# Performance work log

Measured on AMD Instinct MI355X. Metric: run time of the kernel, lower is better.

The kernel has to match this reference:

```python
import jax, jax.numpy as jnp
import numpy as np


def _maxpool2(t):
    # 2x2 max pool, stride 2. t: [B, C, H, W]
    B, C, H, W = t.shape
    return t.reshape(B, C, H // 2, 2, W // 2, 2).max(axis=(3, 5))


def setup_inputs() -> dict:
    key = jax.random.key(0)
    ks = jax.random.split(key, 5)
    B, C, H, W = 4, 64, 128, 128
    x = jax.random.normal(ks[0], (B, C, H, W), dtype=jnp.float32)
    w_theta = jax.random.normal(ks[1], (C // 8, C), dtype=jnp.float32) * (1.0 / np.sqrt(C))
    w_phi = jax.random.normal(ks[2], (C // 8, C), dtype=jnp.float32) * (1.0 / np.sqrt(C))
    w_g = jax.random.normal(ks[3], (C // 2, C), dtype=jnp.float32) * (1.0 / np.sqrt(C))
    w_o = jax.random.normal(ks[4], (C, C // 2), dtype=jnp.float32) * (1.0 / np.sqrt(C // 2))
    gamma = jnp.ones((1,), dtype=jnp.float32)
    return {"x": x, "w_theta": w_theta, "w_phi": w_phi, "w_g": w_g, "w_o": w_o, "gamma": gamma}


def reference(x, w_theta, w_phi, w_g, w_o, gamma):
    B, C, H, W = x.shape
    N = H * W
    # 1x1 convs (bias-free) are channel matmuls
    theta = jnp.einsum('oc,bchw->bohw', w_theta, x)            # [B, C/8, H, W]
    phi = _maxpool2(jnp.einsum('oc,bchw->bohw', w_phi, x))     # [B, C/8, H/2, W/2]
    g = _maxpool2(jnp.einsum('oc,bchw->bohw', w_g, x))         # [B, C/2, H/2, W/2]
    theta = theta.reshape(B, C // 8, N)                        # [B, C/8, N]
    phi = phi.reshape(B, C // 8, N // 4)                       # [B, C/8, N/4]
    g = g.reshape(B, C // 2, N // 4)                           # [B, C/2, N/4]
    # attention: no 1/sqrt(d) scaling in SAGAN
    scores = jnp.einsum('bcn,bcm->bnm', theta, phi)            # [B, N, N/4]
    beta = jax.nn.softmax(scores, axis=-1)
    attn = jnp.einsum('bcm,bnm->bcn', g, beta)                 # [B, C/2, N]
    o = jnp.einsum('oc,bcn->bon', w_o, attn).reshape(B, C, H, W)
    return gamma[0] * o + x
```

## Files before the change

kernel.cpp:

```cpp
#include <hip/hip_runtime.h>
#include <hip/hip_bf16.h>


typedef __attribute__((ext_vector_type(16))) float f32x16;
typedef __attribute__((ext_vector_type(4))) float f32x4;
typedef __attribute__((ext_vector_type(2))) float f32x2;
typedef __attribute__((ext_vector_type(8))) short s16x8;

__device__ __forceinline__ unsigned short f32_bf16(float f) {
    unsigned int u = __float_as_uint(f);
    return (unsigned short)((u + 0x7fffu + ((u >> 16) & 1u)) >> 16);
}
__device__ __forceinline__ unsigned int pk_bf16(float a, float b) {
    return (unsigned int)f32_bf16(a) | ((unsigned int)f32_bf16(b) << 16);
}
__device__ __forceinline__ unsigned int pk_rh(float a, float b) {
    unsigned int au = __float_as_uint(a) + 0x8000u;
    unsigned int bu = __float_as_uint(b) + 0x8000u;
    return __builtin_amdgcn_perm(bu, au, 0x07060302u);
}
__device__ __forceinline__ unsigned int pk_tr(float a, float b) {
    return __builtin_amdgcn_perm(__float_as_uint(b), __float_as_uint(a), 0x07060302u);
}
__device__ __forceinline__ void async16(const void* g, void* l) {
    __builtin_amdgcn_global_load_lds(
        (const __attribute__((address_space(1))) unsigned int*)g,
        (__attribute__((address_space(3))) unsigned int*)l, 16, 0, 0);
}

__global__ __launch_bounds__(256) void proj_kernel(
    const float* __restrict__ x,
    const float* __restrict__ w_theta, const float* __restrict__ w_phi,
    const float* __restrict__ w_g,
    __hip_bfloat16* __restrict__ thG,
    __hip_bfloat16* __restrict__ phG,
    __hip_bfloat16* __restrict__ gG)
{
    __shared__ __align__(16) unsigned short x_s[128 * 72];
    int tid = threadIdx.x;
    int bx = blockIdx.x;
    int b = bx >> 7, mh = (bx >> 1) & 63, ph = bx & 1;

    {
        int cp = tid >> 3, s = tid & 7;
        const float* xb = x + ((size_t)b << 20) + (size_t)(2 * mh) * 128 + 64 * ph;
        const float* p0r = xb + ((size_t)(2 * cp) << 14);
        const float* p1r = p0r + (1 << 14);
#pragma unroll
        for (int py = 0; py < 2; py++)
#pragma unroll
            for (int t = 0; t < 2; t++) {
                int pxl = 4 * s + 32 * t;
                float4 a = *(const float4*)(p0r + py * 128 + pxl);
                float4 c = *(const float4*)(p1r + py * 128 + pxl);
                int pix = py * 64 + pxl;
                *(unsigned int*)&x_s[(pix + 0) * 72 + 2 * cp] = pk_rh(a.x, c.x);
                *(unsigned int*)&x_s[(pix + 1) * 72 + 2 * cp] = pk_rh(a.y, c.y);
                *(unsigned int*)&x_s[(pix + 2) * 72 + 2 * cp] = pk_rh(a.z, c.z);
                *(unsigned int*)&x_s[(pix + 3) * 72 + 2 * cp] = pk_rh(a.w, c.w);
            }
    }

    int lane = tid & 63, w = tid >> 6;
    int q = lane >> 4, nl = lane & 15;

    s16x8 A[3][2];
#pragma unroll
    for (int CT = 0; CT < 3; CT++) {
        const float* wsrc;
        float scale = 1.0f;
        if (CT == 0) {
            if (nl < 8) { wsrc = w_theta + nl * 64; scale = 1.44269504f; }
            else        { wsrc = w_phi + (nl - 8) * 64; }
        } else if (CT == 1) wsrc = w_g + nl * 64;
        else                wsrc = w_g + (16 + nl) * 64;
#pragma unroll
        for (int ks = 0; ks < 2; ks++) {
            const float4* p4 = (const float4*)(wsrc + 32 * ks + 8 * q);
            float4 a0 = p4[0], a1 = p4[1];
            s16x8 f;
            f[0] = (short)f32_bf16(a0.x * scale); f[1] = (short)f32_bf16(a0.y * scale);
            f[2] = (short)f32_bf16(a0.z * scale); f[3] = (short)f32_bf16(a0.w * scale);
            f[4] = (short)f32_bf16(a1.x * scale); f[5] = (short)f32_bf16(a1.y * scale);
            f[6] = (short)f32_bf16(a1.z * scale); f[7] = (short)f32_bf16(a1.w * scale);
            A[CT][ks] = f;
        }
    }
    __syncthreads();

    f32x4 acc[3][2];
#pragma unroll
    for (int ti = 0; ti < 2; ti++) {
        int tile = w + 4 * ti;
        const unsigned short* rb = x_s + (16 * tile + nl) * 72;
        s16x8 B0 = *(const s16x8*)(rb + 8 * q);
        s16x8 B1 = *(const s16x8*)(rb + 32 + 8 * q);
#pragma unroll
        for (int CT = 0; CT < 3; CT++) {
            f32x4 d = (f32x4){0.f, 0.f, 0.f, 0.f};
            d = __builtin_amdgcn_mfma_f32_16x16x32_bf16(A[CT][0], B0, d, 0, 0, 0);
            d = __builtin_amdgcn_mfma_f32_16x16x32_bf16(A[CT][1], B1, d, 0, 0, 0);
            acc[CT][ti] = d;
        }
    }

    if (q < 2) {
        unsigned short* thb = (unsigned short*)thG + ((size_t)b << 14) * 8;
#pragma unroll
        for (int ti = 0; ti < 2; ti++) {
            int n = (2 * mh + ti) * 128 + 64 * ph + 16 * w + nl;
            uint2 tv;
            tv.x = pk_bf16(acc[0][ti][0], acc[0][ti][1]);
            tv.y = pk_bf16(acc[0][ti][2], acc[0][ti][3]);
            *(uint2*)(thb + (size_t)n * 8 + 4 * q) = tv;
        }
    }

    float pool[3][4];
#pragma unroll
    for (int CT = 0; CT < 3; CT++)
#pragma unroll
        for (int r = 0; r < 4; r++) {
            float a = fmaxf(acc[CT][0][r], acc[CT][1][r]);
            pool[CT][r] = fmaxf(a, __shfl_xor(a, 1));
        }

    int mm = 8 * w + (nl >> 1);
    int mbase = mh * 64 + ph * 32;
    if ((nl & 1) == 0) {
        if (q >= 2) {
            uint2 pv;
            pv.x = pk_bf16(pool[0][0], pool[0][1]);
            pv.y = pk_bf16(pool[0][2], pool[0][3]);
            *(uint2*)((unsigned short*)phG + ((size_t)(b * 4096 + mbase + mm)) * 8 + (q - 2) * 4) = pv;
        }
        int p = 16 * ((mm >> 4) & 1) + 8 * ((mm >> 2) & 1) + 4 * ((mm >> 3) & 1) + (mm & 3);
        int mstore = mbase + p;
#pragma unroll
        for (int CT = 1; CT < 3; CT++)
#pragma unroll
            for (int r = 0; r < 4; r++) {
                int cg = 16 * (CT - 1) + 4 * q + r;
                ((unsigned short*)gG)[((size_t)(b * 32 + cg) << 12) + mstore] =
                    f32_bf16(pool[CT][r]);
            }
    }
}

__global__ __launch_bounds__(512, 4) void attn_kernel(
    const __hip_bfloat16* __restrict__ thG, const __hip_bfloat16* __restrict__ phG,
    const __hip_bfloat16* __restrict__ gG,
    const float* __restrict__ w_o, const float* __restrict__ gamma,
    const float* __restrict__ x, float* __restrict__ out)
{
    __shared__ __align__(64) unsigned char smem[40960];

    int tid = threadIdx.x, lane = tid & 63, w = tid >> 6;
    int w4 = w & 3, hf = w >> 2;
    int q = lane >> 4, nl = lane & 15;
    int c31 = lane & 31, h = lane >> 5;
    int bx = blockIdx.x;
    int b  = bx >> 7;
    int n0 = (bx & 127) << 7;
    int nw = n0 + w4 * 32;

    const unsigned short* thb = (const unsigned short*)thG + ((size_t)b << 14) * 8;
    const unsigned short* phb = (const unsigned short*)phG + ((size_t)b << 12) * 8;
    const unsigned short* ggb = (const unsigned short*)gG + ((size_t)b << 17);

    s16x8 BT = (s16x8){0, 0, 0, 0, 0, 0, 0, 0};
    if (h == 0) BT = *(const s16x8*)(thb + (size_t)(nw + c31) * 8);
    else        BT[0] = (short)0xC167;
    s16x8 Fc = (s16x8){0, 0, 0, 0, 0, 0, 0, 0};
    if (h == 1) Fc[0] = (short)0x3F80;

    f32x16 acc = {};
    f32x2  l2 = (f32x2){0.f, 0.f};

    int rA = 8 * w4 + (lane >> 4);
    int rB = rA + 4;
    const unsigned short* gsrcA = ggb + ((size_t)rA << 12) + (hf << 11)
                                  + (((lane & 15) ^ (rA & 15)) << 3);
    const unsigned short* gsrcB = ggb + ((size_t)rB << 12) + (hf << 11)
                                  + (((lane & 15) ^ (rB & 15)) << 3);
    const unsigned short* psrc  = phb + (size_t)((hf << 11) + w4 * 64 + lane) * 8;
    unsigned char* gdst = smem + hf * 16384 + w4 * 2048;
    unsigned char* pdst = smem + 32768 + hf * 4096 + w4 * 1024;

    async16(gsrcA, gdst);
    async16(gsrcB, gdst + 1024);
    if (w4 < 2) async16(psrc, pdst);
    __syncthreads();

    for (int st = 0; st < 16; st++) {
        const unsigned char* gcur = smem + hf * 16384 + (st & 1) * 8192;
        const unsigned char* pcur = smem + 32768 + hf * 4096 + (st & 1) * 2048;
        if (st < 15) {
            int nb = (st + 1) & 1;
            int mo = (st + 1) << 7;
            async16(gsrcA + mo, gdst + nb * 8192);
            async16(gsrcB + mo, gdst + nb * 8192 + 1024);
            if (w4 < 2) async16(psrc + (size_t)mo * 8, pdst + nb * 2048);
        }
#pragma unroll
        for (int t8 = 0; t8 < 4; t8++) {
            int mloc = t8 << 5;
            s16x8 F = Fc;
            if (h == 0) F = *(const s16x8*)(pcur + (mloc + c31) * 16);
            int s0 = (t8 << 2) + h;
            int m15 = c31 & 15;
            s16x8 G1 = *(const s16x8*)(gcur + c31 * 256 + (((s0 + 0) ^ m15) << 4));
            s16x8 G2 = *(const s16x8*)(gcur + c31 * 256 + (((s0 + 2) ^ m15) << 4));

            f32x16 z = {};
            f32x16 S = __builtin_amdgcn_mfma_f32_32x32x16_bf16(F, BT, z, 0, 0, 0);

            float p0  = __builtin_amdgcn_exp2f(S[0]);
            float p1  = __builtin_amdgcn_exp2f(S[1]);
            float p2  = __builtin_amdgcn_exp2f(S[2]);
            float p3  = __builtin_amdgcn_exp2f(S[3]);
            float p4  = __builtin_amdgcn_exp2f(S[4]);
            float p5  = __builtin_amdgcn_exp2f(S[5]);
            float p6  = __builtin_amdgcn_exp2f(S[6]);
            float p7  = __builtin_amdgcn_exp2f(S[7]);
            float p8  = __builtin_amdgcn_exp2f(S[8]);
            float p9  = __builtin_amdgcn_exp2f(S[9]);
            float p10 = __builtin_amdgcn_exp2f(S[10]);
            float p11 = __builtin_amdgcn_exp2f(S[11]);
            float p12 = __builtin_amdgcn_exp2f(S[12]);
            float p13 = __builtin_amdgcn_exp2f(S[13]);
            float p14 = __builtin_amdgcn_exp2f(S[14]);
            float p15 = __builtin_amdgcn_exp2f(S[15]);

            f32x2 u0 = (f32x2){p0, p1} + (f32x2){p2, p3};
            f32x2 u1 = (f32x2){p4, p5} + (f32x2){p6, p7};
            f32x2 u2 = (f32x2){p8, p9} + (f32x2){p10, p11};
            f32x2 u3 = (f32x2){p12, p13} + (f32x2){p14, p15};
            l2 += (u0 + u1) + (u2 + u3);

            uint4 ub1 = make_uint4(pk_tr(p0, p1), pk_tr(p2, p3),
                                   pk_tr(p4, p5), pk_tr(p6, p7));
            uint4 ub2 = make_uint4(pk_tr(p8, p9), pk_tr(p10, p11),
                                   pk_tr(p12, p13), pk_tr(p14, p15));
            s16x8 B1 = *(s16x8*)&ub1;
            s16x8 B2 = *(s16x8*)&ub2;

            acc = __builtin_amdgcn_mfma_f32_32x32x16_bf16(G1, B1, acc, 0, 0, 0);
            acc = __builtin_amdgcn_mfma_f32_32x32x16_bf16(G2, B2, acc, 0, 0, 0);
        }
        __syncthreads();
    }

    float l = l2[0] + l2[1];
    l += __shfl_xor(l, 32);

    int idx = (w4 << 6) + lane;
    if (hf == 1) {
        *(f32x16*)(smem + idx * 64) = acc;
        *(float*)(smem + 32768 + idx * 4) = l;
    }
    __syncthreads();
    if (hf == 0) {
        f32x16 accB = *(const f32x16*)(smem + idx * 64);
        float lB = *(const float*)(smem + 32768 + idx * 4);
        acc += accB;
        float linv = 1.0f / (l + lB);
        acc *= linv;

        s16x8 WO[4];
#pragma unroll
        for (int g4 = 0; g4 < 4; g4++) {
            const float4* wr = (const float4*)(w_o + (size_t)(g4 * 16 + nl) * 32 + q * 8);
            float4 a0 = wr[0], a1 = wr[1];
            WO[g4][0] = (short)f32_bf16(a0.x); WO[g4][1] = (short)f32_bf16(a0.y);
            WO[g4][2] = (short)f32_bf16(a0.z); WO[g4][3] = (short)f32_bf16(a0.w);
            WO[g4][4] = (short)f32_bf16(a1.x); WO[g4][5] = (short)f32_bf16(a1.y);
            WO[g4][6] = (short)f32_bf16(a1.z); WO[g4][7] = (short)f32_bf16(a1.w);
        }
        float gam = gamma[0];

        unsigned char* O_s = smem + 20480;
        int nloc = w4 * 32 + c31;
#pragma unroll
        for (int g2 = 0; g2 < 4; g2++) {
            uint2 ov;
            ov.x = pk_bf16(acc[4 * g2 + 0], acc[4 * g2 + 1]);
            ov.y = pk_bf16(acc[4 * g2 + 2], acc[4 * g2 + 3]);
            *(uint2*)(O_s + nloc * 80 + 16 * g2 + 8 * h) = ov;
        }
        int nloc0 = w4 * 32 + nl;
        int nloc1 = nloc0 + 16;
        s16x8 OB0 = *(const s16x8*)(O_s + nloc0 * 80 + q * 16);
        s16x8 OB1 = *(const s16x8*)(O_s + nloc1 * 80 + q * 16);
#pragma unroll
        for (int g4 = 0; g4 < 4; g4++) {
            f32x4 e0 = (f32x4){0.f, 0.f, 0.f, 0.f};
            f32x4 e1 = (f32x4){0.f, 0.f, 0.f, 0.f};
            e0 = __builtin_amdgcn_mfma_f32_16x16x32_bf16(WO[g4], OB0, e0, 0, 0, 0);
            e1 = __builtin_amdgcn_mfma_f32_16x16x32_bf16(WO[g4], OB1, e1, 0, 0, 0);
#pragma unroll
            for (int r = 0; r < 4; r++) {
                int cc = g4 * 16 + q * 4 + r;
                size_t gi0 = (((size_t)(b * 64 + cc)) << 14) + nw + nl;
                out[gi0] = gam * e0[r] + x[gi0];
                size_t gi1 = gi0 + 16;
                out[gi1] = gam * e1[r] + x[gi1];
            }
        }
    }
}

extern "C" void kernel_launch(void* const* d_in, const int* in_sizes, int n_in,
                              void* d_out, int out_size, void* d_ws, size_t ws_size,
                              hipStream_t stream) {
    const float* x       = (const float*)d_in[0];
    const float* w_theta = (const float*)d_in[1];
    const float* w_phi   = (const float*)d_in[2];
    const float* w_g     = (const float*)d_in[3];
    const float* w_o     = (const float*)d_in[4];
    const float* gamma   = (const float*)d_in[5];
    float* out = (float*)d_out;

    __hip_bfloat16* thG = (__hip_bfloat16*)d_ws;
    __hip_bfloat16* phG = thG + 524288;
    __hip_bfloat16* gG  = phG + 131072;

    proj_kernel<<<512, 256, 0, stream>>>(x, w_theta, w_phi, w_g, thG, phG, gG);
    attn_kernel<<<512, 512, 0, stream>>>(thG, phG, gG, w_o, gamma, x, out);
}
```

Baseline: 117.6 us.

## Split attention key range four ways per block and double grid size

Each attention block now covers 64 query positions instead of 128, using 2 query slices times 4 key-range splits per block. Waves in splits 1 to 3 write partial accumulators and row sums to shared memory, and split 0 reduces them before the output projection. The grid grows to 1024 blocks and the launch bound asks for 8 waves per SIMD, aiming at better occupancy and load balance. The cost is more cross-wave reduction traffic and re-reading theta and weights per block.

```diff
diff --git a/kernel.cpp b/kernel.cpp
--- a/kernel.cpp
+++ b/kernel.cpp
@@ -147,7 +147,7 @@
     }
 }
 
-__global__ __launch_bounds__(512, 4) void attn_kernel(
+__global__ __launch_bounds__(512, 8) void attn_kernel(
     const __hip_bfloat16* __restrict__ thG, const __hip_bfloat16* __restrict__ phG,
     const __hip_bfloat16* __restrict__ gG,
     const float* __restrict__ w_o, const float* __restrict__ gamma,
@@ -156,13 +156,13 @@
     __shared__ __align__(64) unsigned char smem[40960];
 
     int tid = threadIdx.x, lane = tid & 63, w = tid >> 6;
-    int w4 = w & 3, hf = w >> 2;
+    int ns = w & 1, hf = w >> 1;
     int q = lane >> 4, nl = lane & 15;
     int c31 = lane & 31, h = lane >> 5;
     int bx = blockIdx.x;
-    int b  = bx >> 7;
-    int n0 = (bx & 127) << 7;
-    int nw = n0 + w4 * 32;
+    int b  = bx >> 8;
+    int n0 = (bx & 255) << 6;
+    int nw = n0 + ns * 32;
 
     const unsigned short* thb = (const unsigned short*)thG + ((size_t)b << 14) * 8;
     const unsigned short* phb = (const unsigned short*)phG + ((size_t)b << 12) * 8;
@@ -177,40 +177,41 @@
     f32x16 acc = {};
     f32x2  l2 = (f32x2){0.f, 0.f};
 
-    int rA = 8 * w4 + (lane >> 4);
-    int rB = rA + 4;
-    const unsigned short* gsrcA = ggb + ((size_t)rA << 12) + (hf << 11)
-                                  + (((lane & 15) ^ (rA & 15)) << 3);
-    const unsigned short* gsrcB = ggb + ((size_t)rB << 12) + (hf << 11)
-                                  + (((lane & 15) ^ (rB & 15)) << 3);
-    const unsigned short* psrc  = phb + (size_t)((hf << 11) + w4 * 64 + lane) * 8;
-    unsigned char* gdst = smem + hf * 16384 + w4 * 2048;
-    unsigned char* pdst = smem + 32768 + hf * 4096 + w4 * 1024;
-
-    async16(gsrcA, gdst);
-    async16(gsrcB, gdst + 1024);
-    if (w4 < 2) async16(psrc, pdst);
+    int rA = 16 * ns + (lane >> 3);
+    int rB = rA + 8;
+    int wq = hf << 10;
+    const unsigned short* gsrcA = ggb + ((size_t)rA << 12) + wq
+                                  + (((lane & 7) ^ (rA & 7)) << 3);
+    const unsigned short* gsrcB = ggb + ((size_t)rB << 12) + wq
+                                  + (((lane & 7) ^ (rB & 7)) << 3);
+    const unsigned short* psrc  = phb + (size_t)(wq + lane) * 8;
+    unsigned char* gdstA = smem + hf * 4096 + ns * 2048;
+    unsigned char* gdstB = gdstA + 1024;
+    unsigned char* pdst  = smem + 32768 + hf * 1024;
+
+    async16(gsrcA, gdstA);
+    async16(gsrcB, gdstB);
+    if (ns == 0) async16(psrc, pdst);
     __syncthreads();
 
     for (int st = 0; st < 16; st++) {
-        const unsigned char* gcur = smem + hf * 16384 + (st & 1) * 8192;
-        const unsigned char* pcur = smem + 32768 + hf * 4096 + (st & 1) * 2048;
+        const unsigned char* gcur = smem + (st & 1) * 16384 + hf * 4096;
+        const unsigned char* pcur = smem + 32768 + (st & 1) * 4096 + hf * 1024;
         if (st < 15) {
             int nb = (st + 1) & 1;
-            int mo = (st + 1) << 7;
-            async16(gsrcA + mo, gdst + nb * 8192);
-            async16(gsrcB + mo, gdst + nb * 8192 + 1024);
-            if (w4 < 2) async16(psrc + (size_t)mo * 8, pdst + nb * 2048);
-        }
-#pragma unroll
-        for (int t8 = 0; t8 < 4; t8++) {
-            int mloc = t8 << 5;
+            int mo = (st + 1) << 6;
+            async16(gsrcA + mo, gdstA + nb * 16384);
+            async16(gsrcB + mo, gdstB + nb * 16384);
+            if (ns == 0) async16(psrc + (size_t)mo * 8, pdst + nb * 4096);
+        }
+#pragma unroll
+        for (int t8 = 0; t8 < 2; t8++) {
             s16x8 F = Fc;
-            if (h == 0) F = *(const s16x8*)(pcur + (mloc + c31) * 16);
+            if (h == 0) F = *(const s16x8*)(pcur + ((t8 << 5) + c31) * 16);
             int s0 = (t8 << 2) + h;
-            int m15 = c31 & 15;
-            s16x8 G1 = *(const s16x8*)(gcur + c31 * 256 + (((s0 + 0) ^ m15) << 4));
-            s16x8 G2 = *(const s16x8*)(gcur + c31 * 256 + (((s0 + 2) ^ m15) << 4));
+            int m7 = c31 & 7;
+            s16x8 G1 = *(const s16x8*)(gcur + c31 * 128 + (((s0 + 0) ^ m7) << 4));
+            s16x8 G2 = *(const s16x8*)(gcur + c31 * 128 + (((s0 + 2) ^ m7) << 4));
 
             f32x16 z = {};
             f32x16 S = __builtin_amdgcn_mfma_f32_32x32x16_bf16(F, BT, z, 0, 0, 0);
@@ -254,17 +255,20 @@
     float l = l2[0] + l2[1];
     l += __shfl_xor(l, 32);
 
-    int idx = (w4 << 6) + lane;
-    if (hf == 1) {
-        *(f32x16*)(smem + idx * 64) = acc;
-        *(float*)(smem + 32768 + idx * 4) = l;
+    if (hf != 0) {
+        int reg = (hf - 1) * 2 + ns;
+        *(f32x16*)(smem + reg * 5120 + lane * 80) = acc;
+        *(float*)(smem + 30720 + reg * 256 + lane * 4) = l;
     }
     __syncthreads();
     if (hf == 0) {
-        f32x16 accB = *(const f32x16*)(smem + idx * 64);
-        float lB = *(const float*)(smem + 32768 + idx * 4);
-        acc += accB;
-        float linv = 1.0f / (l + lB);
+#pragma unroll
+        for (int k = 0; k < 3; k++) {
+            int reg = k * 2 + ns;
+            acc += *(const f32x16*)(smem + reg * 5120 + lane * 80);
+            l += *(const float*)(smem + 30720 + reg * 256 + lane * 4);
+        }
+        float linv = 1.0f / l;
         acc *= linv;
 
         s16x8 WO[4];
@@ -279,8 +283,8 @@
         }
         float gam = gamma[0];
 
-        unsigned char* O_s = smem + 20480;
-        int nloc = w4 * 32 + c31;
+        unsigned char* O_s = smem + 34816;
+        int nloc = ns * 32 + c31;
 #pragma unroll
         for (int g2 = 0; g2 < 4; g2++) {
             uint2 ov;
@@ -288,7 +292,7 @@
             ov.y = pk_bf16(acc[4 * g2 + 2], acc[4 * g2 + 3]);
             *(uint2*)(O_s + nloc * 80 + 16 * g2 + 8 * h) = ov;
         }
-        int nloc0 = w4 * 32 + nl;
+        int nloc0 = ns * 32 + nl;
         int nloc1 = nloc0 + 16;
         s16x8 OB0 = *(const s16x8*)(O_s + nloc0 * 80 + q * 16);
         s16x8 OB1 = *(const s16x8*)(O_s + nloc1 * 80 + q * 16);
@@ -326,5 +330,5 @@
     __hip_bfloat16* gG  = phG + 131072;
 
     proj_kernel<<<512, 256, 0, stream>>>(x, w_theta, w_phi, w_g, thG, phG, gG);
-    attn_kernel<<<512, 512, 0, stream>>>(thG, phG, gG, w_o, gamma, x, out);
-}
+    attn_kernel<<<1024, 512, 0, stream>>>(thG, phG, gG, w_o, gamma, x, out);
+}
```

Result: slower. 128.1 us (+9.0%).
